# Kernel optimization log

Hardware: AMD Instinct MI355X
Metric: run time of the kernel (lower is better)

The kernel has to match this reference:

```python
import jax, jax.numpy as jnp
import numpy as np
from jax import lax

DIM = 256; RESO = 64; STRIPE = 8; NH = 8
HSP, WSP = RESO, STRIPE   # attention_mode=0: vertical stripes
HD = DIM // NH
B = 8; L = RESO * RESO
WIN = HSP * WSP           # tokens per window (512)


def _vertical_mask():
    # Faithful to verticalAttnMask: column labels 0/1/2 over last stripe, then
    # window-partition and pairwise-compare.
    shift = STRIPE // 2
    lab = np.zeros(RESO, np.float32)
    lab[RESO - STRIPE:RESO - shift] = 1.0
    lab[RESO - shift:] = 2.0
    img = np.broadcast_to(lab[None, :], (RESO, RESO))            # [H, W]
    # shiftedWindowVerticalPartition with reso=RESO, stripes=STRIPE
    mw = img.reshape(RESO, RESO // STRIPE, STRIPE).transpose(1, 0, 2).reshape(-1, WIN)
    diff = mw[:, None, :] - mw[:, :, None]                        # [nW, L, L]
    return jnp.asarray(np.where(diff != 0.0, -100.0, 0.0).astype(np.float32))

_MASK = _vertical_mask()  # [nW=8, 512, 512]


def _seq2cswin(x):
    Bx = x.shape[0]
    img = x.transpose(0, 2, 1).reshape(Bx, DIM, RESO, RESO)
    w = img.reshape(Bx, DIM, RESO // HSP, HSP, RESO // WSP, WSP)
    w = w.transpose(0, 2, 4, 3, 5, 1).reshape(-1, WIN, DIM)
    return w.reshape(-1, WIN, NH, HD).transpose(0, 2, 1, 3)


def _forward(qkv, scale, proj_w, proj_b, conv_w, conv_b):
    q, k, v = qkv[0], qkv[1], qkv[2]
    qw = _seq2cswin(q) * scale[0]
    kw = _seq2cswin(k)
    # get_lepe: window-partition v as images, depthwise 3x3 conv
    vimg = v.transpose(0, 2, 1).reshape(B, DIM, RESO, RESO)
    vwin = vimg.reshape(B, DIM, RESO // HSP, HSP, RESO // WSP, WSP)
    vwin = vwin.transpose(0, 2, 4, 1, 3, 5).reshape(-1, DIM, HSP, WSP)  # [B*nW, C, Hsp, Wsp]
    lepe = lax.conv_general_dilated(
        vwin, conv_w, (1, 1), ((1, 1), (1, 1)),
        dimension_numbers=('NCHW', 'OIHW', 'NCHW'), feature_group_count=DIM
    ) + conv_b[None, :, None, None]
    lepe = lepe.reshape(-1, NH, HD, WIN).transpose(0, 1, 3, 2)
    vw = vwin.reshape(-1, NH, HD, WIN).transpose(0, 1, 3, 2)
    attn = jnp.einsum('wnid,wnjd->wnij', qw, kw)
    # currentDepth odd, mode 0 -> vertical shifted-window mask
    attn = attn + jnp.tile(_MASK, (B, 1, 1))[:, None, :, :]
    attn = jax.nn.softmax(attn, axis=-1)
    x = jnp.einsum('wnij,wnjd->wnid', attn, vw) + lepe
    x = x.transpose(0, 2, 1, 3).reshape(-1, WIN, DIM)
    x = x @ proj_w.T + proj_b
    # CSwin2img then flatten back to [B, L, C]
    x = x.reshape(B, RESO // HSP, RESO // WSP, HSP, WSP, DIM)
    x = x.transpose(0, 1, 3, 2, 4, 5).reshape(B, RESO, RESO, DIM)
    return x.reshape(B, L, DIM)


def setup_inputs() -> dict:
    key = jax.random.key(0)
    ks = jax.random.split(key, 5)
    qkv = jax.random.normal(ks[0], (3, B, L, DIM), jnp.float32)
    scale = jnp.full((1,), HD ** (-0.5), jnp.float32)
    proj_w = jax.random.normal(ks[1], (DIM, DIM), jnp.float32) * (DIM ** -0.5)
    proj_b = jax.random.normal(ks[2], (DIM,), jnp.float32) * 0.02
    conv_w = jax.random.normal(ks[3], (DIM, 1, 3, 3), jnp.float32) * 0.1
    conv_b = jax.random.normal(ks[4], (DIM,), jnp.float32) * 0.02
    return {"qkv": qkv, "scale": scale, "proj_w": proj_w, "proj_b": proj_b,
            "conv_w": conv_w, "conv_b": conv_b}


def reference(qkv, scale, proj_w, proj_b, conv_w, conv_b):
    return _forward(qkv, scale, proj_w, proj_b, conv_w, conv_b)
```

## Files before the change

kernel.cpp:

```cpp
#include <hip/hip_runtime.h>
#include <hip/hip_bf16.h>

#define BATCH 8
#define NH    8
#define HD    32
#define WIN   512
#define DIM   256
#define RESO  64
#define SEQL  4096
#define VSTRIDE 520
#define WPAD  264

#define LOG2E 1.44269504088896340736f

extern "C" __device__ float __ocml_native_exp2_f32(float);

typedef __attribute__((ext_vector_type(8))) short short8;
typedef __attribute__((ext_vector_type(4))) float floatx4;

__device__ __forceinline__ unsigned short f2bf(float f) {
    union { float f; unsigned int i; } x; x.f = f;
    unsigned int r = x.i + 0x7fff + ((x.i >> 16) & 1);
    return (unsigned short)(r >> 16);
}
__device__ __forceinline__ float bf2f(unsigned short u) {
    union { unsigned int i; float f; } x; x.i = ((unsigned int)u) << 16; return x.f;
}
__device__ __forceinline__ unsigned int pk2(float lo, float hi) {
    return ((unsigned int)f2bf(hi) << 16) | (unsigned int)f2bf(lo);
}
__device__ __forceinline__ unsigned int pk2t(float lo, float hi) {
    union { float f; unsigned int i; } a, b; a.f = lo; b.f = hi;
    return __builtin_amdgcn_perm(b.i, a.i, 0x07060302);
}
__device__ __forceinline__ void unp2(unsigned int u, float& lo, float& hi) {
    union { unsigned int i; float f; } a, b;
    a.i = u << 16; b.i = u & 0xffff0000u;
    lo = a.f; hi = b.f;
}

union FragU {
    unsigned int  u[4];
    unsigned short us[8];
    short8        s;
    ushort4       v4[2];
};

__global__ __launch_bounds__(512, 4)
void attn_mfma_kernel(const float* __restrict__ qkv,
                      const float* __restrict__ scale_p,
                      const float* __restrict__ conv_w,
                      const float* __restrict__ conv_b,
                      unsigned short* __restrict__ X)
{
    __shared__ alignas(16) unsigned short Klds[WIN * HD];
    __shared__ alignas(16) unsigned short Vt[HD * VSTRIDE];
    __shared__ float cw[HD * 9];
    __shared__ float cb[HD];

    const int wh   = blockIdx.x;
    const int bw   = wh >> 3;
    const int head = wh & 7;
    const int b    = bw >> 3;
    const int wx   = bw & 7;
    const int tid  = threadIdx.x;

    const float scale = scale_p[0] * LOG2E;
    const size_t plane = (size_t)BATCH * SEQL * DIM;
    const float* qg = qkv;
    const float* kg = qkv + plane;
    const float* vg = qkv + 2 * plane;

    for (int idx = tid; idx < WIN * 4; idx += 512) {
        const int t = idx >> 2, c8 = idx & 3;
        const size_t goff = ((size_t)b * SEQL + (size_t)(t >> 3) * RESO + wx * 8 + (t & 7)) * DIM
                          + head * HD + c8 * 8;
        const float4 k0 = *(const float4*)(kg + goff);
        const float4 k1 = *(const float4*)(kg + goff + 4);
        uint4 pk;
        pk.x = pk2t(k0.x, k0.y); pk.y = pk2t(k0.z, k0.w);
        pk.z = pk2t(k1.x, k1.y); pk.w = pk2t(k1.z, k1.w);
        const int p = c8 ^ ((t >> 1) & 3);
        *(uint4*)&Klds[t * HD + p * 8] = pk;
    }
    for (int idx = tid; idx < 256 * HD; idx += 512) {
        const int ch = idx & 31, tp = idx >> 5;
        const int t = tp * 2;
        const size_t goff = ((size_t)b * SEQL + (size_t)(t >> 3) * RESO + wx * 8 + (t & 7)) * DIM
                          + head * HD + ch;
        const float v0 = vg[goff];
        const float v1 = vg[goff + DIM];
        *(unsigned int*)&Vt[ch * VSTRIDE + t] = pk2(v0, v1);
    }
    for (int i = tid; i < HD * 9; i += 512) cw[i] = conv_w[head * HD * 9 + i];
    if (tid < HD) cb[tid] = conv_b[head * HD + tid];
    __syncthreads();

    const int lane = tid & 63, wid = tid >> 6;
    const int q4 = lane >> 4, nn = lane & 15;
    const int qbase = wid * 64;
    const bool mwin = (wx == 7);

    float mk[4];
    #pragma unroll
    for (int r = 0; r < 4; ++r) {
        const bool kgrp = (((q4 * 4 + r) & 7) < 4);
        const bool qgrp = ((nn & 7) < 4);
        mk[r] = (kgrp != qgrp) ? (-100.f * LOG2E) : 0.f;
    }

    short8 qf[4];
    #pragma unroll
    for (int qq = 0; qq < 4; ++qq) {
        const int t = qbase + qq * 16 + nn;
        const size_t goff = ((size_t)b * SEQL + (size_t)(t >> 3) * RESO + wx * 8 + (t & 7)) * DIM
                          + head * HD + q4 * 8;
        const float4 a = *(const float4*)(qg + goff);
        const float4 c = *(const float4*)(qg + goff + 4);
        FragU f;
        f.u[0] = pk2t(a.x * scale, a.y * scale);
        f.u[1] = pk2t(a.z * scale, a.w * scale);
        f.u[2] = pk2t(c.x * scale, c.y * scale);
        f.u[3] = pk2t(c.z * scale, c.w * scale);
        qf[qq] = f.s;
    }

    floatx4 acc[4][2];
    #pragma unroll
    for (int qq = 0; qq < 4; ++qq) {
        acc[qq][0] = (floatx4){0.f, 0.f, 0.f, 0.f};
        acc[qq][1] = (floatx4){0.f, 0.f, 0.f, 0.f};
    }
    float rs[4] = {0.f, 0.f, 0.f, 0.f};
    const floatx4 zf = (floatx4){0.f, 0.f, 0.f, 0.f};

    for (int kc = 0; kc < 16; ++kc) {
        short8 kf0, kf1;
        {
            const int t0 = (2 * kc) * 16 + nn;
            const int t1 = (2 * kc + 1) * 16 + nn;
            kf0 = *(const short8*)&Klds[t0 * HD + (q4 ^ ((t0 >> 1) & 3)) * 8];
            kf1 = *(const short8*)&Klds[t1 * HD + (q4 ^ ((t1 >> 1) & 3)) * 8];
        }
        short8 vf[2];
        #pragma unroll
        for (int nt = 0; nt < 2; ++nt) {
            const int ch = nt * 16 + nn;
            FragU f;
            f.v4[0] = *(const ushort4*)&Vt[ch * VSTRIDE + kc * 32 + q4 * 4];
            f.v4[1] = *(const ushort4*)&Vt[ch * VSTRIDE + kc * 32 + 16 + q4 * 4];
            vf[nt] = f.s;
        }
        #pragma unroll
        for (int qq = 0; qq < 4; ++qq) {
            floatx4 s0 = __builtin_amdgcn_mfma_f32_16x16x32_bf16(kf0, qf[qq], zf, 0, 0, 0);
            floatx4 s1 = __builtin_amdgcn_mfma_f32_16x16x32_bf16(kf1, qf[qq], zf, 0, 0, 0);
            if (mwin) {
                #pragma unroll
                for (int r = 0; r < 4; ++r) { s0[r] += mk[r]; s1[r] += mk[r]; }
            }
            float p[8];
            #pragma unroll
            for (int r = 0; r < 4; ++r) {
                p[r]     = __ocml_native_exp2_f32(s0[r]);
                p[4 + r] = __ocml_native_exp2_f32(s1[r]);
            }
            rs[qq] += ((p[0] + p[1]) + (p[2] + p[3])) + ((p[4] + p[5]) + (p[6] + p[7]));
            FragU pf;
            pf.u[0] = pk2t(p[0], p[1]);
            pf.u[1] = pk2t(p[2], p[3]);
            pf.u[2] = pk2t(p[4], p[5]);
            pf.u[3] = pk2t(p[6], p[7]);
            acc[qq][0] = __builtin_amdgcn_mfma_f32_16x16x32_bf16(vf[0], pf.s, acc[qq][0], 0, 0, 0);
            acc[qq][1] = __builtin_amdgcn_mfma_f32_16x16x32_bf16(vf[1], pf.s, acc[qq][1], 0, 0, 0);
        }
    }

    float inv[4];
    #pragma unroll
    for (int qq = 0; qq < 4; ++qq) {
        float v = rs[qq];
        v += __shfl_xor(v, 16);
        v += __shfl_xor(v, 32);
        inv[qq] = 1.0f / v;
    }

    #pragma unroll
    for (int qq = 0; qq < 4; ++qq) {
        const int t = qbase + qq * 16 + nn;
        const int h = t >> 3, wi = t & 7;
        #pragma unroll
        for (int nt = 0; nt < 2; ++nt) {
            const int chb = nt * 16 + q4 * 4;
            float o[4];
            #pragma unroll
            for (int r = 0; r < 4; ++r)
                o[r] = acc[qq][nt][r] * inv[qq] + cb[chb + r];
            #pragma unroll
            for (int dh = -1; dh <= 1; ++dh) {
                const int hh = h + dh;
                if (hh < 0 || hh >= RESO) continue;
                #pragma unroll
                for (int dw = -1; dw <= 1; ++dw) {
                    const int ww = wi + dw;
                    if (ww < 0 || ww >= 8) continue;
                    const int tj  = hh * 8 + ww;
                    const int wof = (dh + 1) * 3 + (dw + 1);
                    #pragma unroll
                    for (int r = 0; r < 4; ++r)
                        o[r] += cw[(chb + r) * 9 + wof] * bf2f(Vt[(chb + r) * VSTRIDE + tj]);
                }
            }
            ushort4 st;
            st.x = f2bf(o[0]); st.y = f2bf(o[1]); st.z = f2bf(o[2]); st.w = f2bf(o[3]);
            *(ushort4*)&X[((size_t)bw * WIN + t) * DIM + head * HD + chb] = st;
        }
    }
}

__global__ __launch_bounds__(256, 4)
void proj_mfma_kernel(const unsigned short* __restrict__ X,
                      const float* __restrict__ pw,
                      const float* __restrict__ pb,
                      float* __restrict__ out)
{
    __shared__ alignas(16) unsigned short Wl[64 * WPAD];

    const int bx   = blockIdx.x;
    const int mblk = bx >> 2;
    const int nblk = bx & 3;
    const int tid  = threadIdx.x;
    const int n0   = nblk * 64;

    {
        const int row = tid >> 2;
        const int cb0 = (tid & 3) * 64;
        #pragma unroll
        for (int c = 0; c < 64; c += 8) {
            const float4 w0 = *(const float4*)&pw[(size_t)(n0 + row) * DIM + cb0 + c];
            const float4 w1 = *(const float4*)&pw[(size_t)(n0 + row) * DIM + cb0 + c + 4];
            uint4 pk;
            pk.x = pk2(w0.x, w0.y); pk.y = pk2(w0.z, w0.w);
            pk.z = pk2(w1.x, w1.y); pk.w = pk2(w1.z, w1.w);
            *(uint4*)&Wl[row * WPAD + cb0 + c] = pk;
        }
    }
    __syncthreads();

    const int lane = tid & 63, wid = tid >> 6;
    const int q4 = lane >> 4, nn = lane & 15;
    const int mwave = mblk * 256 + wid * 64;

    floatx4 acc[4][4];
    #pragma unroll
    for (int i = 0; i < 4; ++i)
        #pragma unroll
        for (int j = 0; j < 4; ++j)
            acc[i][j] = (floatx4){0.f, 0.f, 0.f, 0.f};

    for (int kk = 0; kk < 8; ++kk) {
        short8 af[4], bf[4];
        #pragma unroll
        for (int nt = 0; nt < 4; ++nt)
            af[nt] = *(const short8*)&Wl[(nt * 16 + nn) * WPAD + kk * 32 + q4 * 8];
        #pragma unroll
        for (int mt = 0; mt < 4; ++mt) {
            const int m = mwave + mt * 16 + nn;
            bf[mt] = *(const short8*)&X[(size_t)m * DIM + kk * 32 + q4 * 8];
        }
        #pragma unroll
        for (int nt = 0; nt < 4; ++nt)
            #pragma unroll
            for (int mt = 0; mt < 4; ++mt)
                acc[nt][mt] = __builtin_amdgcn_mfma_f32_16x16x32_bf16(af[nt], bf[mt], acc[nt][mt], 0, 0, 0);
    }

    float4 bias[4];
    #pragma unroll
    for (int nt = 0; nt < 4; ++nt)
        bias[nt] = *(const float4*)&pb[n0 + nt * 16 + q4 * 4];

    size_t rowoff[4];
    #pragma unroll
    for (int mt = 0; mt < 4; ++mt) {
        const int m  = mwave + mt * 16 + nn;
        const int bw = m >> 9, t = m & 511;
        const int bb = bw >> 3, wx = bw & 7, hh = t >> 3, wi = t & 7;
        rowoff[mt] = ((size_t)bb * SEQL + (size_t)hh * RESO + wx * 8 + wi) * DIM;
    }

    #pragma unroll
    for (int nt = 0; nt < 4; ++nt)
        #pragma unroll
        for (int mt = 0; mt < 4; ++mt) {
            float4 v;
            v.x = acc[nt][mt][0] + bias[nt].x;
            v.y = acc[nt][mt][1] + bias[nt].y;
            v.z = acc[nt][mt][2] + bias[nt].z;
            v.w = acc[nt][mt][3] + bias[nt].w;
            *(float4*)&out[rowoff[mt] + n0 + nt * 16 + q4 * 4] = v;
        }
}

extern "C" void kernel_launch(void* const* d_in, const int* in_sizes, int n_in,
                              void* d_out, int out_size, void* d_ws, size_t ws_size,
                              hipStream_t stream)
{
    const float* qkv    = (const float*)d_in[0];
    const float* scale  = (const float*)d_in[1];
    const float* proj_w = (const float*)d_in[2];
    const float* proj_b = (const float*)d_in[3];
    const float* conv_w = (const float*)d_in[4];
    const float* conv_b = (const float*)d_in[5];

    unsigned short* X = (unsigned short*)d_ws;

    attn_mfma_kernel<<<dim3(BATCH * NH * 8), dim3(512), 0, stream>>>(
        qkv, scale, conv_w, conv_b, X);

    proj_mfma_kernel<<<dim3(512), dim3(256), 0, stream>>>(
        X, proj_w, proj_b, (float*)d_out);
}
```

Baseline: 213.5 us.

## Read LePE conv inputs from global fp32, vectorize V staging and transpose conv weights

The depthwise 3x3 LePE conv now loads V neighbours straight from global memory as float4 and reads weights from a transposed LDS table as float4, instead of scalar bf16 reads from the transposed V tile. It also precomputes the conv in fp32 rather than bf16-rounded V. V staging into LDS switches from scalar paired loads to float4 loads with scalar bf16 stores, and the stride changes to 522 to reduce bank conflicts. The projection k-loop is fully unrolled. The global neighbour reads rely on L2 hits and may add memory latency to the epilogue.

```diff
diff --git a/kernel.cpp b/kernel.cpp
--- a/kernel.cpp
+++ b/kernel.cpp
@@ -8,7 +8,7 @@
 #define DIM   256
 #define RESO  64
 #define SEQL  4096
-#define VSTRIDE 520
+#define VSTRIDE 522
 #define WPAD  264
 
 #define LOG2E 1.44269504088896340736f
@@ -22,9 +22,6 @@
     union { float f; unsigned int i; } x; x.f = f;
     unsigned int r = x.i + 0x7fff + ((x.i >> 16) & 1);
     return (unsigned short)(r >> 16);
-}
-__device__ __forceinline__ float bf2f(unsigned short u) {
-    union { unsigned int i; float f; } x; x.i = ((unsigned int)u) << 16; return x.f;
 }
 __device__ __forceinline__ unsigned int pk2(float lo, float hi) {
     return ((unsigned int)f2bf(hi) << 16) | (unsigned int)f2bf(lo);
@@ -55,7 +52,7 @@
 {
     __shared__ alignas(16) unsigned short Klds[WIN * HD];
     __shared__ alignas(16) unsigned short Vt[HD * VSTRIDE];
-    __shared__ float cw[HD * 9];
+    __shared__ alignas(16) float cwT[9 * HD];
     __shared__ float cb[HD];
 
     const int wh   = blockIdx.x;
@@ -83,16 +80,26 @@
         const int p = c8 ^ ((t >> 1) & 3);
         *(uint4*)&Klds[t * HD + p * 8] = pk;
     }
-    for (int idx = tid; idx < 256 * HD; idx += 512) {
-        const int ch = idx & 31, tp = idx >> 5;
-        const int t = tp * 2;
+    for (int idx = tid; idx < WIN * 4; idx += 512) {
+        const int t = idx & 511, seg = idx >> 9;
         const size_t goff = ((size_t)b * SEQL + (size_t)(t >> 3) * RESO + wx * 8 + (t & 7)) * DIM
-                          + head * HD + ch;
-        const float v0 = vg[goff];
-        const float v1 = vg[goff + DIM];
-        *(unsigned int*)&Vt[ch * VSTRIDE + t] = pk2(v0, v1);
-    }
-    for (int i = tid; i < HD * 9; i += 512) cw[i] = conv_w[head * HD * 9 + i];
+                          + head * HD + seg * 8;
+        const float4 v0 = *(const float4*)(vg + goff);
+        const float4 v1 = *(const float4*)(vg + goff + 4);
+        const int ch0 = seg * 8;
+        Vt[(ch0 + 0) * VSTRIDE + t] = f2bf(v0.x);
+        Vt[(ch0 + 1) * VSTRIDE + t] = f2bf(v0.y);
+        Vt[(ch0 + 2) * VSTRIDE + t] = f2bf(v0.z);
+        Vt[(ch0 + 3) * VSTRIDE + t] = f2bf(v0.w);
+        Vt[(ch0 + 4) * VSTRIDE + t] = f2bf(v1.x);
+        Vt[(ch0 + 5) * VSTRIDE + t] = f2bf(v1.y);
+        Vt[(ch0 + 6) * VSTRIDE + t] = f2bf(v1.z);
+        Vt[(ch0 + 7) * VSTRIDE + t] = f2bf(v1.w);
+    }
+    if (tid < 9 * HD) {
+        const int wof = tid >> 5, ch = tid & 31;
+        cwT[wof * HD + ch] = conv_w[head * HD * 9 + ch * 9 + wof];
+    }
     if (tid < HD) cb[tid] = conv_b[head * HD + tid];
     __syncthreads();
 
@@ -189,30 +196,43 @@
     for (int qq = 0; qq < 4; ++qq) {
         const int t = qbase + qq * 16 + nn;
         const int h = t >> 3, wi = t & 7;
+        float o[2][4];
         #pragma unroll
         for (int nt = 0; nt < 2; ++nt) {
             const int chb = nt * 16 + q4 * 4;
-            float o[4];
             #pragma unroll
             for (int r = 0; r < 4; ++r)
-                o[r] = acc[qq][nt][r] * inv[qq] + cb[chb + r];
+                o[nt][r] = acc[qq][nt][r] * inv[qq] + cb[chb + r];
+        }
+        #pragma unroll
+        for (int dh = -1; dh <= 1; ++dh) {
+            const int hh = h + dh;
+            if (hh < 0 || hh >= RESO) continue;
             #pragma unroll
-            for (int dh = -1; dh <= 1; ++dh) {
-                const int hh = h + dh;
-                if (hh < 0 || hh >= RESO) continue;
+            for (int dw = -1; dw <= 1; ++dw) {
+                const int ww = wi + dw;
+                if (ww < 0 || ww >= 8) continue;
+                const int wof = (dh + 1) * 3 + (dw + 1);
+                const size_t gv = ((size_t)b * SEQL + (size_t)hh * RESO + wx * 8 + ww) * DIM
+                                + head * HD;
                 #pragma unroll
-                for (int dw = -1; dw <= 1; ++dw) {
-                    const int ww = wi + dw;
-                    if (ww < 0 || ww >= 8) continue;
-                    const int tj  = hh * 8 + ww;
-                    const int wof = (dh + 1) * 3 + (dw + 1);
-                    #pragma unroll
-                    for (int r = 0; r < 4; ++r)
-                        o[r] += cw[(chb + r) * 9 + wof] * bf2f(Vt[(chb + r) * VSTRIDE + tj]);
+                for (int nt = 0; nt < 2; ++nt) {
+                    const int chb = nt * 16 + q4 * 4;
+                    const float4 vv = *(const float4*)(vg + gv + chb);
+                    const float4 wv = *(const float4*)&cwT[wof * HD + chb];
+                    o[nt][0] += wv.x * vv.x;
+                    o[nt][1] += wv.y * vv.y;
+                    o[nt][2] += wv.z * vv.z;
+                    o[nt][3] += wv.w * vv.w;
                 }
             }
+        }
+        #pragma unroll
+        for (int nt = 0; nt < 2; ++nt) {
+            const int chb = nt * 16 + q4 * 4;
             ushort4 st;
-            st.x = f2bf(o[0]); st.y = f2bf(o[1]); st.z = f2bf(o[2]); st.w = f2bf(o[3]);
+            st.x = f2bf(o[nt][0]); st.y = f2bf(o[nt][1]);
+            st.z = f2bf(o[nt][2]); st.w = f2bf(o[nt][3]);
             *(ushort4*)&X[((size_t)bw * WIN + t) * DIM + head * HD + chb] = st;
         }
     }
@@ -258,6 +278,7 @@
         for (int j = 0; j < 4; ++j)
             acc[i][j] = (floatx4){0.f, 0.f, 0.f, 0.f};
 
+    #pragma unroll
     for (int kk = 0; kk < 8; ++kk) {
         short8 af[4], bf[4];
         #pragma unroll
```

Result: slower. 222.5 us (+4.2%).
